# Kernel tuning notes

Measured on AMD Instinct MI355X. Metric: run time of the kernel, lower is better.

## Reference

```python
import jax, jax.numpy as jnp
import numpy as np

B, S, H = 8, 4096, 512
I = 1024
E = 8
TOP_K = 2


def setup_inputs() -> dict:
    key = jax.random.key(0)
    k1, k2, k3, k4, k5 = jax.random.split(key, 5)
    scale_h = 1.0 / np.sqrt(H)
    scale_i = 1.0 / np.sqrt(I)
    return {
        "hidden_states": jax.random.normal(k1, (B, S, H), dtype=jnp.float32),
        "w_router": jax.random.normal(k2, (E, H), dtype=jnp.float32) * scale_h,
        "w_gate": jax.random.normal(k3, (E, I, H), dtype=jnp.float32) * scale_h,
        "w_up": jax.random.normal(k4, (E, I, H), dtype=jnp.float32) * scale_h,
        "w_down": jax.random.normal(k5, (E, H, I), dtype=jnp.float32) * scale_i,
    }


def reference(hidden_states, w_router, w_gate, w_up, w_down):
    dt = hidden_states.dtype
    # Router: logits [B,S,E]
    router_logits = jnp.einsum("bsh,eh->bse", hidden_states, w_router)
    top_vals, top_idx = jax.lax.top_k(router_logits, TOP_K)  # [B,S,K]
    top_w = jax.nn.softmax(top_vals, axis=-1)                # [B,S,K]
    # one-hot over experts: [B,S,K,E]
    oh = jax.nn.one_hot(top_idx, E, dtype=dt)
    combine = jnp.einsum("bsk,bske->bse", top_w, oh)         # per-expert weight per token

    # Faithful to the original: every expert processes the full token batch,
    # result is weighted by the (mostly-zero) combine weights.
    output = jnp.zeros_like(hidden_states)
    for e in range(E):  # fixed small expert count
        g = jnp.einsum("bsh,ih->bsi", hidden_states, w_gate[e])
        u = jnp.einsum("bsh,ih->bsi", hidden_states, w_up[e])
        eo = jnp.einsum("bsi,hi->bsh", jax.nn.silu(g) * u, w_down[e])
        output = output + eo * combine[..., e][..., None]

    # Aux load-balancing loss
    router_probs = jax.nn.softmax(router_logits, axis=-1).mean(axis=(0, 1))  # [E]
    usage = oh.sum(axis=(0, 1, 2))                                           # counts [E]
    usage = usage / jnp.maximum(usage.sum(), 1.0)
    aux_loss = (router_probs * usage).sum() * float(E)
    return output, aux_loss
```

## Files before the change

kernel.cpp:

```cpp
#include <hip/hip_runtime.h>
#include <hip/hip_bf16.h>
#include <math.h>

#define Bb 8
#define Ss 4096
#define Hh 512
#define Ii 1024
#define Ee 8
#define NTOK (Bb*Ss)
#define TT 32
#define IC 128
#define KS 16
#define NBUCKET 64


#define FMA4(acc, s, b) { (acc).x += (s)*(b).x; (acc).y += (s)*(b).y; (acc).z += (s)*(b).z; (acc).w += (s)*(b).w; }

__device__ __forceinline__ float silu_f(float g) {
    return g / (1.0f + expf(-g));
}

__global__ __launch_bounds__(256) void router_kernel(
    const float* __restrict__ hs, const float* __restrict__ wr,
    int* __restrict__ cnt, float* __restrict__ probs_part,
    int* __restrict__ ttok, float* __restrict__ twt)
{
    __shared__ __align__(16) float swr[Ee*Hh];
    __shared__ float sblk[Ee];
    int tid = threadIdx.x;
    for (int q = tid; q < Ee*Hh/4; q += 256)
        ((float4*)swr)[q] = ((const float4*)wr)[q];
    if (tid < Ee) sblk[tid] = 0.0f;
    __syncthreads();

    int lane = tid & 63;
    int t = blockIdx.x*4 + (tid >> 6);
    const float4* h4 = (const float4*)(hs + (size_t)t*Hh);

    float acc[Ee];
    #pragma unroll
    for (int e = 0; e < Ee; e++) acc[e] = 0.0f;
    #pragma unroll
    for (int r = 0; r < 2; r++) {
        float4 hv = h4[lane + 64*r];
        #pragma unroll
        for (int e = 0; e < Ee; e++) {
            float4 wv = ((const float4*)swr)[e*(Hh/4) + lane + 64*r];
            acc[e] += hv.x*wv.x + hv.y*wv.y + hv.z*wv.z + hv.w*wv.w;
        }
    }
    #pragma unroll
    for (int e = 0; e < Ee; e++) {
        #pragma unroll
        for (int off = 32; off > 0; off >>= 1)
            acc[e] += __shfl_xor(acc[e], off);
    }

    if (lane == 0) {
        float m = acc[0];
        #pragma unroll
        for (int e = 1; e < Ee; e++) m = fmaxf(m, acc[e]);
        float p[Ee], s = 0.0f;
        #pragma unroll
        for (int e = 0; e < Ee; e++) { p[e] = expf(acc[e]-m); s += p[e]; }
        float inv = 1.0f/s;
        #pragma unroll
        for (int e = 0; e < Ee; e++) atomicAdd(&sblk[e], p[e]*inv);

        int e0 = 0; float v0 = acc[0];
        #pragma unroll
        for (int e = 1; e < Ee; e++) if (acc[e] > v0) { v0 = acc[e]; e0 = e; }
        int e1 = -1; float v1 = -1e30f;
        #pragma unroll
        for (int e = 0; e < Ee; e++) if (e != e0 && acc[e] > v1) { v1 = acc[e]; e1 = e; }
        float r1 = expf(v1 - v0);
        float w0 = 1.0f/(1.0f + r1);
        float w1 = r1*w0;
        int p0 = atomicAdd(&cnt[e0], 1);
        ttok[e0*NTOK + p0] = t; twt[e0*NTOK + p0] = w0;
        int p1 = atomicAdd(&cnt[e1], 1);
        ttok[e1*NTOK + p1] = t; twt[e1*NTOK + p1] = w1;
    }
    __syncthreads();
    if (tid < Ee)
        atomicAdd(&probs_part[(blockIdx.x & (NBUCKET-1))*Ee + tid], sblk[tid]);
}

__global__ void aux_kernel(const int* __restrict__ cnt,
                           const float* __restrict__ probs_part,
                           float* __restrict__ out_aux)
{
    if (threadIdx.x == 0 && blockIdx.x == 0) {
        float aux = 0.0f;
        for (int e = 0; e < Ee; e++) {
            float ps = 0.0f;
            for (int b = 0; b < NBUCKET; b++) ps += probs_part[b*Ee + e];
            aux += (ps/(float)NTOK) * ((float)cnt[e]/(float)(2*NTOK));
        }
        out_aux[0] = aux * (float)Ee;
    }
}

__global__ __launch_bounds__(256)
__attribute__((amdgpu_waves_per_eu(1, 3)))
void expert_kernel(
    const float* __restrict__ hs,
    const float* __restrict__ wg, const float* __restrict__ wu,
    const float* __restrict__ wd,
    const int* __restrict__ cnt, const int* __restrict__ ttok,
    const float* __restrict__ twt,
    float* __restrict__ out)
{
    int e  = blockIdx.x & (Ee-1);
    int bx = blockIdx.x >> 3;
    int n = cnt[e];
    int j0 = bx * TT;
    if (j0 >= n) return;

    __shared__ __align__(16) float smem[IC*TT + KS*Hh];
    __shared__ int   sm_tok[TT];
    __shared__ float sm_wt[TT];
    float* sm_act = smem;
    float* sm_hT  = smem + IC*TT;
    float* sm_wgT = smem + IC*TT + KS*TT;
    float* sm_wuT = smem + IC*TT + KS*TT + KS*IC;
    float* sm_wdT = smem + IC*TT;

    int tid = threadIdx.x;
    if (tid < TT) {
        int j = j0 + tid;
        int tk; float w;
        if (j < n) { tk = ttok[e*NTOK + j]; w = twt[e*NTOK + j]; }
        else       { tk = ttok[e*NTOK + j0]; w = 0.0f; }
        sm_tok[tid] = tk; sm_wt[tid] = w;
    }
    __syncthreads();

    const float* wg_e = wg + (size_t)e*Ii*Hh;
    const float* wu_e = wu + (size_t)e*Ii*Hh;
    const float* wd_e = wd + (size_t)e*Hh*Ii;

    int t0 = (tid >> 5) * 4;
    int x0 = (tid & 31) * 4;

    int t_h = (tid >> 2) & (TT-1);
    int kq  = (tid & 3) << 2;
    const float* hrow_base = hs + (size_t)sm_tok[t_h]*Hh + kq;
    float* sm_hT_st = sm_hT + kq*TT + t_h;
    int il = tid & 127;
    int kb = (tid >> 7) << 3;
    float* sm_wgT_st = sm_wgT + kb*IC + il;
    float* sm_wuT_st = sm_wuT + kb*IC + il;
    int hh = tid << 1;
    const float* wd_row0 = wd_e + (size_t)hh*Ii;
    const float* wd_row1 = wd_row0 + Ii;
    float* sm_wdT_st = sm_wdT + hh;

    float4 acc_out[4][4];
    #pragma unroll
    for (int a = 0; a < 4; a++)
        #pragma unroll
        for (int b = 0; b < 4; b++)
            acc_out[a][b] = make_float4(0.f, 0.f, 0.f, 0.f);

    for (int ic = 0; ic < Ii; ic += IC) {
        float4 accg[4], accu[4];
        #pragma unroll
        for (int a = 0; a < 4; a++) { accg[a] = make_float4(0,0,0,0); accu[a] = make_float4(0,0,0,0); }

        const float* hp = hrow_base;
        const float* gp = wg_e + (size_t)(ic + il)*Hh + kb;
        const float* up = wu_e + (size_t)(ic + il)*Hh + kb;

        float4 hv = make_float4(0,0,0,0), g0, g1, u0, u1;
        if (tid < 128) hv = *(const float4*)hp;
        g0 = *(const float4*)gp;       g1 = *(const float4*)(gp + 4);
        u0 = *(const float4*)up;       u1 = *(const float4*)(up + 4);

        for (int ks = 0; ks < Hh; ks += KS) {
            if (tid < 128) {
                sm_hT_st[0*TT] = hv.x; sm_hT_st[1*TT] = hv.y;
                sm_hT_st[2*TT] = hv.z; sm_hT_st[3*TT] = hv.w;
            }
            sm_wgT_st[0*IC] = g0.x; sm_wgT_st[1*IC] = g0.y;
            sm_wgT_st[2*IC] = g0.z; sm_wgT_st[3*IC] = g0.w;
            sm_wgT_st[4*IC] = g1.x; sm_wgT_st[5*IC] = g1.y;
            sm_wgT_st[6*IC] = g1.z; sm_wgT_st[7*IC] = g1.w;
            sm_wuT_st[0*IC] = u0.x; sm_wuT_st[1*IC] = u0.y;
            sm_wuT_st[2*IC] = u0.z; sm_wuT_st[3*IC] = u0.w;
            sm_wuT_st[4*IC] = u1.x; sm_wuT_st[5*IC] = u1.y;
            sm_wuT_st[6*IC] = u1.z; sm_wuT_st[7*IC] = u1.w;
            __syncthreads();

            if (ks + KS < Hh) {
                hp += KS; gp += KS; up += KS;
                if (tid < 128) hv = *(const float4*)hp;
                g0 = *(const float4*)gp;   g1 = *(const float4*)(gp + 4);
                u0 = *(const float4*)up;   u1 = *(const float4*)(up + 4);
            }

            #pragma unroll
            for (int k = 0; k < KS; k++) {
                float4 a  = *(const float4*)&sm_hT [k*TT + t0];
                float4 bg = *(const float4*)&sm_wgT[k*IC + x0];
                float4 bu = *(const float4*)&sm_wuT[k*IC + x0];
                FMA4(accg[0], a.x, bg); FMA4(accg[1], a.y, bg);
                FMA4(accg[2], a.z, bg); FMA4(accg[3], a.w, bg);
                FMA4(accu[0], a.x, bu); FMA4(accu[1], a.y, bu);
                FMA4(accu[2], a.z, bu); FMA4(accu[3], a.w, bu);
            }
            __syncthreads();
        }

        {
            float4 v;
            v.x = silu_f(accg[0].x)*accu[0].x; v.y = silu_f(accg[1].x)*accu[1].x;
            v.z = silu_f(accg[2].x)*accu[2].x; v.w = silu_f(accg[3].x)*accu[3].x;
            *(float4*)&sm_act[(x0+0)*TT + t0] = v;
            v.x = silu_f(accg[0].y)*accu[0].y; v.y = silu_f(accg[1].y)*accu[1].y;
            v.z = silu_f(accg[2].y)*accu[2].y; v.w = silu_f(accg[3].y)*accu[3].y;
            *(float4*)&sm_act[(x0+1)*TT + t0] = v;
            v.x = silu_f(accg[0].z)*accu[0].z; v.y = silu_f(accg[1].z)*accu[1].z;
            v.z = silu_f(accg[2].z)*accu[2].z; v.w = silu_f(accg[3].z)*accu[3].z;
            *(float4*)&sm_act[(x0+2)*TT + t0] = v;
            v.x = silu_f(accg[0].w)*accu[0].w; v.y = silu_f(accg[1].w)*accu[1].w;
            v.z = silu_f(accg[2].w)*accu[2].w; v.w = silu_f(accg[3].w)*accu[3].w;
            *(float4*)&sm_act[(x0+3)*TT + t0] = v;
        }
        __syncthreads();

        float4 c0[2][4];
        {
            const float* s0 = wd_row0 + ic;
            const float* s1 = wd_row1 + ic;
            #pragma unroll
            for (int q = 0; q < 4; q++) {
                c0[0][q] = *(const float4*)(s0 + 4*q);
                c0[1][q] = *(const float4*)(s1 + 4*q);
            }
        }
        for (int ks2 = 0; ks2 < IC; ks2 += KS) {
            #pragma unroll
            for (int rr = 0; rr < 2; rr++) {
                float* st = sm_wdT_st + rr;
                st[ 0*Hh] = c0[rr][0].x; st[ 1*Hh] = c0[rr][0].y;
                st[ 2*Hh] = c0[rr][0].z; st[ 3*Hh] = c0[rr][0].w;
                st[ 4*Hh] = c0[rr][1].x; st[ 5*Hh] = c0[rr][1].y;
                st[ 6*Hh] = c0[rr][1].z; st[ 7*Hh] = c0[rr][1].w;
                st[ 8*Hh] = c0[rr][2].x; st[ 9*Hh] = c0[rr][2].y;
                st[10*Hh] = c0[rr][2].z; st[11*Hh] = c0[rr][2].w;
                st[12*Hh] = c0[rr][3].x; st[13*Hh] = c0[rr][3].y;
                st[14*Hh] = c0[rr][3].z; st[15*Hh] = c0[rr][3].w;
            }
            __syncthreads();

            if (ks2 + KS < IC) {
                const float* s0 = wd_row0 + ic + ks2 + KS;
                const float* s1 = wd_row1 + ic + ks2 + KS;
                #pragma unroll
                for (int q = 0; q < 4; q++) {
                    c0[0][q] = *(const float4*)(s0 + 4*q);
                    c0[1][q] = *(const float4*)(s1 + 4*q);
                }
            }

            #pragma unroll
            for (int k = 0; k < KS; k++) {
                float4 av = *(const float4*)&sm_act[(ks2+k)*TT + t0];
                #pragma unroll
                for (int j = 0; j < 4; j++) {
                    float4 b = *(const float4*)&sm_wdT[k*Hh + x0 + 128*j];
                    FMA4(acc_out[0][j], av.x, b);
                    FMA4(acc_out[1][j], av.y, b);
                    FMA4(acc_out[2][j], av.z, b);
                    FMA4(acc_out[3][j], av.w, b);
                }
            }
            __syncthreads();
        }
    }

    #pragma unroll
    for (int tj = 0; tj < 4; tj++) {
        float w = sm_wt[t0 + tj];
        size_t base = (size_t)sm_tok[t0 + tj]*Hh;
        #pragma unroll
        for (int j = 0; j < 4; j++) {
            float4 v = acc_out[tj][j];
            atomicAdd(&out[base + x0 + 128*j + 0], v.x*w);
            atomicAdd(&out[base + x0 + 128*j + 1], v.y*w);
            atomicAdd(&out[base + x0 + 128*j + 2], v.z*w);
            atomicAdd(&out[base + x0 + 128*j + 3], v.w*w);
        }
    }
}

extern "C" void kernel_launch(void* const* d_in, const int* in_sizes, int n_in,
                              void* d_out, int out_size, void* d_ws, size_t ws_size,
                              hipStream_t stream) {
    const float* hs = (const float*)d_in[0];
    const float* wr = (const float*)d_in[1];
    const float* wg = (const float*)d_in[2];
    const float* wu = (const float*)d_in[3];
    const float* wd = (const float*)d_in[4];
    float* out = (float*)d_out;

    int*   cnt   = (int*)d_ws;
    float* probs = (float*)((char*)d_ws + 64);
    int*   ttok  = (int*)((char*)d_ws + 4096);
    float* twt   = (float*)((char*)d_ws + 4096 + sizeof(int)*(size_t)Ee*NTOK);

    hipMemsetAsync(d_out, 0, (size_t)(NTOK*Hh + 1)*sizeof(float), stream);
    hipMemsetAsync(d_ws, 0, 4096, stream);

    router_kernel<<<NTOK/4, 256, 0, stream>>>(hs, wr, cnt, probs, ttok, twt);
    aux_kernel<<<1, 64, 0, stream>>>(cnt, probs, out + (size_t)NTOK*Hh);

    int tiles = (NTOK + TT - 1)/TT;
    expert_kernel<<<tiles*Ee, 256, 0, stream>>>(hs, wg, wu, wd, cnt, ttok, twt, out);
}
```

Baseline: 5.189 ms.

## Replace FP32 FMA expert path with split-bf16 MFMA grouped GEMMs

Splits the activations and the expert weights into hi/lo bf16 planes and runs the expert FFN as two grouped GEMM kernels built on 32x32x16 bf16 MFMA. Each product uses three MFMAs (hi*hi, lo*hi, hi*lo) to approximate fp32 accuracy. The intermediate silu(g)*u activations go to a padded, per-expert-prefixed workspace buffer instead of being recomputed inside a fused kernel. The aim is to move the matmul work off scalar FP32 FMAs and onto the matrix cores. The cost is extra split passes over the weights every call, a large workspace, and an activation round-trip through global memory, with a fallback to the old kernel when the workspace is too small.

```diff
diff --git a/kernel.cpp b/kernel.cpp
--- a/kernel.cpp
+++ b/kernel.cpp
@@ -8,11 +8,42 @@
 #define Ii 1024
 #define Ee 8
 #define NTOK (Bb*Ss)
+#define NBUCKET 64
+
 #define TT 32
 #define IC 128
 #define KS 16
-#define NBUCKET 64
-
+
+#define BM 64
+#define BN 256
+#define BK 32
+#define LDK 40
+
+typedef short  bf16x8 __attribute__((ext_vector_type(8)));
+typedef float  f32x16 __attribute__((ext_vector_type(16)));
+#define MFMA32(a,b,c) __builtin_amdgcn_mfma_f32_32x32x16_bf16((a),(b),(c),0,0,0)
+#define ZERO16 {0.f,0.f,0.f,0.f,0.f,0.f,0.f,0.f,0.f,0.f,0.f,0.f,0.f,0.f,0.f,0.f}
+
+#define WS_CNT     0
+#define WS_PROBS   64
+#define WS_PREFIX  4096
+#define WS_TTOK    8192ull
+#define WS_TWT     (WS_TTOK + 4ull*Ee*NTOK)
+#define WS_PLANES  (WS_TWT + 4ull*Ee*NTOK)
+#define HS_N   ((size_t)NTOK*Hh)
+#define WE_N   ((size_t)Ee*Ii*Hh)
+#define WS_HS_HI   WS_PLANES
+#define WS_HS_LO   (WS_HS_HI + 2ull*HS_N)
+#define WS_WG_HI   (WS_HS_LO + 2ull*HS_N)
+#define WS_WG_LO   (WS_WG_HI + 2ull*WE_N)
+#define WS_WU_HI   (WS_WG_LO + 2ull*WE_N)
+#define WS_WU_LO   (WS_WU_HI + 2ull*WE_N)
+#define WS_WD_HI   (WS_WU_LO + 2ull*WE_N)
+#define WS_WD_LO   (WS_WD_HI + 2ull*WE_N)
+#define ACT_ROWS   66560ull
+#define WS_ACT_HI  (WS_WD_LO + 2ull*WE_N)
+#define WS_ACT_LO  (WS_ACT_HI + 2ull*ACT_ROWS*Ii)
+#define WS_NEED    (WS_ACT_LO + 2ull*ACT_ROWS*Ii)
 
 #define FMA4(acc, s, b) { (acc).x += (s)*(b).x; (acc).y += (s)*(b).y; (acc).z += (s)*(b).z; (acc).w += (s)*(b).w; }
 
@@ -88,16 +119,320 @@
 
 __global__ void aux_kernel(const int* __restrict__ cnt,
                            const float* __restrict__ probs_part,
-                           float* __restrict__ out_aux)
+                           float* __restrict__ out_aux,
+                           int* __restrict__ prefix)
 {
     if (threadIdx.x == 0 && blockIdx.x == 0) {
         float aux = 0.0f;
+        int acc = 0;
         for (int e = 0; e < Ee; e++) {
             float ps = 0.0f;
             for (int b = 0; b < NBUCKET; b++) ps += probs_part[b*Ee + e];
             aux += (ps/(float)NTOK) * ((float)cnt[e]/(float)(2*NTOK));
+            prefix[e] = acc;
+            acc += ((cnt[e] + 63) >> 6) << 6;
         }
         out_aux[0] = aux * (float)Ee;
+        prefix[8] = acc;
+    }
+}
+
+__global__ __launch_bounds__(256) void split_kernel(
+    const float* __restrict__ src, ushort* __restrict__ hi, ushort* __restrict__ lo, int n4)
+{
+    int idx = blockIdx.x*256 + threadIdx.x;
+    if (idx >= n4) return;
+    float4 f = ((const float4*)src)[idx];
+    ushort h[4], l[4];
+    #pragma unroll
+    for (int j = 0; j < 4; j++) {
+        float fv = ((const float*)&f)[j];
+        unsigned u = __float_as_uint(fv);
+        unsigned r = (u + 0x7fffu + ((u>>16)&1u)) & 0xffff0000u;
+        h[j] = (ushort)(r >> 16);
+        float lof = fv - __uint_as_float(r);
+        l[j] = (ushort)(__float_as_uint(lof) >> 16);
+    }
+    ((ushort4*)hi)[idx] = make_ushort4(h[0], h[1], h[2], h[3]);
+    ((ushort4*)lo)[idx] = make_ushort4(l[0], l[1], l[2], l[3]);
+}
+
+__global__ __launch_bounds__(256)
+__attribute__((amdgpu_waves_per_eu(1, 2)))
+void gemm1_kernel(const ushort* __restrict__ hs_hi, const ushort* __restrict__ hs_lo,
+                  const ushort* __restrict__ wg_hi, const ushort* __restrict__ wg_lo,
+                  const ushort* __restrict__ wu_hi, const ushort* __restrict__ wu_lo,
+                  const int* __restrict__ cnt, const int* __restrict__ prefix,
+                  const int* __restrict__ ttok,
+                  ushort* __restrict__ act_hi, ushort* __restrict__ act_lo)
+{
+    const int e  = blockIdx.x & 7;
+    const int rr = blockIdx.x >> 3;
+    const int mt = rr & 511;
+    const int it = rr >> 9;
+    const int n  = cnt[e];
+    const int j0 = mt * BM;
+    if (j0 >= n) return;
+    const int abase = prefix[e] + j0;
+    const int ic = it * 128;
+
+    __shared__ __align__(16) ushort sA[2][BM*LDK];
+    __shared__ __align__(16) ushort sB[2][BN*LDK];
+    __shared__ int sm_tok[BM];
+
+    const int tid = threadIdx.x;
+    if (tid < BM) {
+        int j = j0 + tid;
+        sm_tok[tid] = ttok[e*NTOK + (j < n ? j : j0)];
+    }
+    __syncthreads();
+
+    const int srow = tid >> 2;
+    const int sch  = tid & 3;
+    const int sxch = (sch ^ ((srow >> 3) & 3)) * 8;
+    const ushort* aph = hs_hi + (size_t)sm_tok[srow]*Hh + sch*8;
+    const ushort* apl = hs_lo + (size_t)sm_tok[srow]*Hh + sch*8;
+    const int a_st = srow*LDK + sxch;
+
+    const ushort* wgh_e = wg_hi + (size_t)e*Ii*Hh;
+    const ushort* wgl_e = wg_lo + (size_t)e*Ii*Hh;
+    const ushort* wuh_e = wu_hi + (size_t)e*Ii*Hh;
+    const ushort* wul_e = wu_lo + (size_t)e*Ii*Hh;
+    const ushort* bph[4];
+    const ushort* bpl[4];
+    bph[0] = wgh_e + (size_t)(ic +      srow)*Hh + sch*8;
+    bpl[0] = wgl_e + (size_t)(ic +      srow)*Hh + sch*8;
+    bph[1] = wgh_e + (size_t)(ic + 64 + srow)*Hh + sch*8;
+    bpl[1] = wgl_e + (size_t)(ic + 64 + srow)*Hh + sch*8;
+    bph[2] = wuh_e + (size_t)(ic +      srow)*Hh + sch*8;
+    bpl[2] = wul_e + (size_t)(ic +      srow)*Hh + sch*8;
+    bph[3] = wuh_e + (size_t)(ic + 64 + srow)*Hh + sch*8;
+    bpl[3] = wul_e + (size_t)(ic + 64 + srow)*Hh + sch*8;
+    int b_st[4];
+    #pragma unroll
+    for (int c = 0; c < 4; c++) b_st[c] = (c*64 + srow)*LDK + sxch;
+
+    const int w   = tid >> 6;
+    const int l31 = tid & 31;
+    const int g   = (tid >> 5) & 1;
+    const int axr = (l31 >> 3) & 3;
+    const int ck0 = ((g    ) ^ axr) * 8;
+    const int ck1 = ((g + 2) ^ axr) * 8;
+    const int arow0 = (     l31)*LDK;
+    const int arow1 = (32 + l31)*LDK;
+    const int brow_g = ((w  )*32 + l31)*LDK;
+    const int brow_u = ((w+4)*32 + l31)*LDK;
+
+    f32x16 accg0 = ZERO16, accg1 = ZERO16, accu0 = ZERO16, accu1 = ZERO16;
+
+    bf16x8 ra_h = *(const bf16x8*)aph;
+    bf16x8 ra_l = *(const bf16x8*)apl;
+    bf16x8 rb_h[4], rb_l[4];
+    #pragma unroll
+    for (int c = 0; c < 4; c++) { rb_h[c] = *(const bf16x8*)bph[c]; rb_l[c] = *(const bf16x8*)bpl[c]; }
+
+    for (int ks = 0; ks < Hh/BK; ks++) {
+        *(bf16x8*)&sA[0][a_st] = ra_h;
+        *(bf16x8*)&sA[1][a_st] = ra_l;
+        #pragma unroll
+        for (int c = 0; c < 4; c++) {
+            *(bf16x8*)&sB[0][b_st[c]] = rb_h[c];
+            *(bf16x8*)&sB[1][b_st[c]] = rb_l[c];
+        }
+        __syncthreads();
+
+        if (ks + 1 < Hh/BK) {
+            aph += BK; apl += BK;
+            ra_h = *(const bf16x8*)aph; ra_l = *(const bf16x8*)apl;
+            #pragma unroll
+            for (int c = 0; c < 4; c++) {
+                bph[c] += BK; bpl[c] += BK;
+                rb_h[c] = *(const bf16x8*)bph[c];
+                rb_l[c] = *(const bf16x8*)bpl[c];
+            }
+        }
+
+        #pragma unroll
+        for (int kk = 0; kk < 2; kk++) {
+            const int ck = kk ? ck1 : ck0;
+            bf16x8 a0h = *(const bf16x8*)&sA[0][arow0 + ck];
+            bf16x8 a0l = *(const bf16x8*)&sA[1][arow0 + ck];
+            bf16x8 a1h = *(const bf16x8*)&sA[0][arow1 + ck];
+            bf16x8 a1l = *(const bf16x8*)&sA[1][arow1 + ck];
+            bf16x8 bgh = *(const bf16x8*)&sB[0][brow_g + ck];
+            bf16x8 bgl = *(const bf16x8*)&sB[1][brow_g + ck];
+            bf16x8 buh = *(const bf16x8*)&sB[0][brow_u + ck];
+            bf16x8 bul = *(const bf16x8*)&sB[1][brow_u + ck];
+            accg0 = MFMA32(a0h, bgh, accg0);
+            accg0 = MFMA32(a0l, bgh, accg0);
+            accg0 = MFMA32(a0h, bgl, accg0);
+            accu0 = MFMA32(a0h, buh, accu0);
+            accu0 = MFMA32(a0l, buh, accu0);
+            accu0 = MFMA32(a0h, bul, accu0);
+            accg1 = MFMA32(a1h, bgh, accg1);
+            accg1 = MFMA32(a1l, bgh, accg1);
+            accg1 = MFMA32(a1h, bgl, accg1);
+            accu1 = MFMA32(a1h, buh, accu1);
+            accu1 = MFMA32(a1l, buh, accu1);
+            accu1 = MFMA32(a1h, bul, accu1);
+        }
+        __syncthreads();
+    }
+
+    const int icol = ic + w*32 + l31;
+    #pragma unroll
+    for (int r = 0; r < 16; r++) {
+        int m = (r&3) + 8*(r>>2) + 4*g;
+        {
+            float a = silu_f(accg0[r]) * accu0[r];
+            size_t off = (size_t)(abase + m)*Ii + icol;
+            unsigned u = __float_as_uint(a);
+            unsigned rh = (u + 0x7fffu + ((u>>16)&1u)) & 0xffff0000u;
+            act_hi[off] = (ushort)(rh >> 16);
+            float lof = a - __uint_as_float(rh);
+            act_lo[off] = (ushort)(__float_as_uint(lof) >> 16);
+        }
+        {
+            float a = silu_f(accg1[r]) * accu1[r];
+            size_t off = (size_t)(abase + 32 + m)*Ii + icol;
+            unsigned u = __float_as_uint(a);
+            unsigned rh = (u + 0x7fffu + ((u>>16)&1u)) & 0xffff0000u;
+            act_hi[off] = (ushort)(rh >> 16);
+            float lof = a - __uint_as_float(rh);
+            act_lo[off] = (ushort)(__float_as_uint(lof) >> 16);
+        }
+    }
+}
+
+__global__ __launch_bounds__(256)
+__attribute__((amdgpu_waves_per_eu(1, 2)))
+void gemm2_kernel(const ushort* __restrict__ act_hi, const ushort* __restrict__ act_lo,
+                  const ushort* __restrict__ wd_hi, const ushort* __restrict__ wd_lo,
+                  const int* __restrict__ cnt, const int* __restrict__ prefix,
+                  const int* __restrict__ ttok, const float* __restrict__ twt,
+                  float* __restrict__ out)
+{
+    const int e  = blockIdx.x & 7;
+    const int rr = blockIdx.x >> 3;
+    const int mt = rr & 511;
+    const int ht = rr >> 9;
+    const int n  = cnt[e];
+    const int j0 = mt * BM;
+    if (j0 >= n) return;
+    const int abase = prefix[e] + j0;
+    const int hbase = ht * 256;
+
+    __shared__ __align__(16) ushort sA[2][BM*LDK];
+    __shared__ __align__(16) ushort sB[2][BN*LDK];
+    __shared__ int   sm_tok[BM];
+    __shared__ float sm_wt[BM];
+
+    const int tid = threadIdx.x;
+    if (tid < BM) {
+        int j = j0 + tid;
+        if (j < n) { sm_tok[tid] = ttok[e*NTOK + j]; sm_wt[tid] = twt[e*NTOK + j]; }
+        else       { sm_tok[tid] = ttok[e*NTOK + j0]; sm_wt[tid] = 0.0f; }
+    }
+    __syncthreads();
+
+    const int srow = tid >> 2;
+    const int sch  = tid & 3;
+    const int sxch = (sch ^ ((srow >> 3) & 3)) * 8;
+    const ushort* aph = act_hi + (size_t)(abase + srow)*Ii + sch*8;
+    const ushort* apl = act_lo + (size_t)(abase + srow)*Ii + sch*8;
+    const int a_st = srow*LDK + sxch;
+
+    const ushort* wdh_e = wd_hi + (size_t)e*Hh*Ii;
+    const ushort* wdl_e = wd_lo + (size_t)e*Hh*Ii;
+    const ushort* bph[4];
+    const ushort* bpl[4];
+    #pragma unroll
+    for (int c = 0; c < 4; c++) {
+        bph[c] = wdh_e + (size_t)(hbase + c*64 + srow)*Ii + sch*8;
+        bpl[c] = wdl_e + (size_t)(hbase + c*64 + srow)*Ii + sch*8;
+    }
+    int b_st[4];
+    #pragma unroll
+    for (int c = 0; c < 4; c++) b_st[c] = (c*64 + srow)*LDK + sxch;
+
+    const int w   = tid >> 6;
+    const int l31 = tid & 31;
+    const int g   = (tid >> 5) & 1;
+    const int axr = (l31 >> 3) & 3;
+    const int ck0 = ((g    ) ^ axr) * 8;
+    const int ck1 = ((g + 2) ^ axr) * 8;
+    const int arow0 = (     l31)*LDK;
+    const int arow1 = (32 + l31)*LDK;
+    const int brow_a = ((w  )*32 + l31)*LDK;
+    const int brow_b = ((w+4)*32 + l31)*LDK;
+
+    f32x16 acc00 = ZERO16, acc01 = ZERO16, acc10 = ZERO16, acc11 = ZERO16;
+
+    bf16x8 ra_h = *(const bf16x8*)aph;
+    bf16x8 ra_l = *(const bf16x8*)apl;
+    bf16x8 rb_h[4], rb_l[4];
+    #pragma unroll
+    for (int c = 0; c < 4; c++) { rb_h[c] = *(const bf16x8*)bph[c]; rb_l[c] = *(const bf16x8*)bpl[c]; }
+
+    for (int ks = 0; ks < Ii/BK; ks++) {
+        *(bf16x8*)&sA[0][a_st] = ra_h;
+        *(bf16x8*)&sA[1][a_st] = ra_l;
+        #pragma unroll
+        for (int c = 0; c < 4; c++) {
+            *(bf16x8*)&sB[0][b_st[c]] = rb_h[c];
+            *(bf16x8*)&sB[1][b_st[c]] = rb_l[c];
+        }
+        __syncthreads();
+
+        if (ks + 1 < Ii/BK) {
+            aph += BK; apl += BK;
+            ra_h = *(const bf16x8*)aph; ra_l = *(const bf16x8*)apl;
+            #pragma unroll
+            for (int c = 0; c < 4; c++) {
+                bph[c] += BK; bpl[c] += BK;
+                rb_h[c] = *(const bf16x8*)bph[c];
+                rb_l[c] = *(const bf16x8*)bpl[c];
+            }
+        }
+
+        #pragma unroll
+        for (int kk = 0; kk < 2; kk++) {
+            const int ck = kk ? ck1 : ck0;
+            bf16x8 a0h = *(const bf16x8*)&sA[0][arow0 + ck];
+            bf16x8 a0l = *(const bf16x8*)&sA[1][arow0 + ck];
+            bf16x8 a1h = *(const bf16x8*)&sA[0][arow1 + ck];
+            bf16x8 a1l = *(const bf16x8*)&sA[1][arow1 + ck];
+            bf16x8 b0h = *(const bf16x8*)&sB[0][brow_a + ck];
+            bf16x8 b0l = *(const bf16x8*)&sB[1][brow_a + ck];
+            bf16x8 b1h = *(const bf16x8*)&sB[0][brow_b + ck];
+            bf16x8 b1l = *(const bf16x8*)&sB[1][brow_b + ck];
+            acc00 = MFMA32(a0h, b0h, acc00);
+            acc00 = MFMA32(a0l, b0h, acc00);
+            acc00 = MFMA32(a0h, b0l, acc00);
+            acc01 = MFMA32(a0h, b1h, acc01);
+            acc01 = MFMA32(a0l, b1h, acc01);
+            acc01 = MFMA32(a0h, b1l, acc01);
+            acc10 = MFMA32(a1h, b0h, acc10);
+            acc10 = MFMA32(a1l, b0h, acc10);
+            acc10 = MFMA32(a1h, b0l, acc10);
+            acc11 = MFMA32(a1h, b1h, acc11);
+            acc11 = MFMA32(a1l, b1h, acc11);
+            acc11 = MFMA32(a1h, b1l, acc11);
+        }
+        __syncthreads();
+    }
+
+    const int h0 = hbase +       w*32 + l31;
+    const int h1 = hbase + 128 + w*32 + l31;
+    #pragma unroll
+    for (int r = 0; r < 16; r++) {
+        int m = (r&3) + 8*(r>>2) + 4*g;
+        int   tok0 = sm_tok[m],      tok1 = sm_tok[32 + m];
+        float wt0  = sm_wt[m],       wt1  = sm_wt[32 + m];
+        atomicAdd(&out[(size_t)tok0*Hh + h0], acc00[r]*wt0);
+        atomicAdd(&out[(size_t)tok0*Hh + h1], acc01[r]*wt0);
+        atomicAdd(&out[(size_t)tok1*Hh + h0], acc10[r]*wt1);
+        atomicAdd(&out[(size_t)tok1*Hh + h1], acc11[r]*wt1);
     }
 }
 
@@ -241,16 +576,16 @@
         }
         for (int ks2 = 0; ks2 < IC; ks2 += KS) {
             #pragma unroll
-            for (int rr = 0; rr < 2; rr++) {
-                float* st = sm_wdT_st + rr;
-                st[ 0*Hh] = c0[rr][0].x; st[ 1*Hh] = c0[rr][0].y;
-                st[ 2*Hh] = c0[rr][0].z; st[ 3*Hh] = c0[rr][0].w;
-                st[ 4*Hh] = c0[rr][1].x; st[ 5*Hh] = c0[rr][1].y;
-                st[ 6*Hh] = c0[rr][1].z; st[ 7*Hh] = c0[rr][1].w;
-                st[ 8*Hh] = c0[rr][2].x; st[ 9*Hh] = c0[rr][2].y;
-                st[10*Hh] = c0[rr][2].z; st[11*Hh] = c0[rr][2].w;
-                st[12*Hh] = c0[rr][3].x; st[13*Hh] = c0[rr][3].y;
-                st[14*Hh] = c0[rr][3].z; st[15*Hh] = c0[rr][3].w;
+            for (int rr2 = 0; rr2 < 2; rr2++) {
+                float* st = sm_wdT_st + rr2;
+                st[ 0*Hh] = c0[rr2][0].x; st[ 1*Hh] = c0[rr2][0].y;
+                st[ 2*Hh] = c0[rr2][0].z; st[ 3*Hh] = c0[rr2][0].w;
+                st[ 4*Hh] = c0[rr2][1].x; st[ 5*Hh] = c0[rr2][1].y;
+                st[ 6*Hh] = c0[rr2][1].z; st[ 7*Hh] = c0[rr2][1].w;
+                st[ 8*Hh] = c0[rr2][2].x; st[ 9*Hh] = c0[rr2][2].y;
+                st[10*Hh] = c0[rr2][2].z; st[11*Hh] = c0[rr2][2].w;
+                st[12*Hh] = c0[rr2][3].x; st[13*Hh] = c0[rr2][3].y;
+                st[14*Hh] = c0[rr2][3].z; st[15*Hh] = c0[rr2][3].w;
             }
             __syncthreads();
 
@@ -305,17 +640,41 @@
     const float* wd = (const float*)d_in[4];
     float* out = (float*)d_out;
 
-    int*   cnt   = (int*)d_ws;
-    float* probs = (float*)((char*)d_ws + 64);
-    int*   ttok  = (int*)((char*)d_ws + 4096);
-    float* twt   = (float*)((char*)d_ws + 4096 + sizeof(int)*(size_t)Ee*NTOK);
-
-    hipMemsetAsync(d_out, 0, (size_t)(NTOK*Hh + 1)*sizeof(float), stream);
-    hipMemsetAsync(d_ws, 0, 4096, stream);
+    char* ws = (char*)d_ws;
+    int*   cnt    = (int*)(ws + WS_CNT);
+    float* probs  = (float*)(ws + WS_PROBS);
+    int*   prefix = (int*)(ws + WS_PREFIX);
+    int*   ttok   = (int*)(ws + WS_TTOK);
+    float* twt    = (float*)(ws + WS_TWT);
+
+    hipMemsetAsync(d_out, 0, ((size_t)NTOK*Hh + 1)*sizeof(float), stream);
+    hipMemsetAsync(d_ws, 0, 4608, stream);
 
     router_kernel<<<NTOK/4, 256, 0, stream>>>(hs, wr, cnt, probs, ttok, twt);
-    aux_kernel<<<1, 64, 0, stream>>>(cnt, probs, out + (size_t)NTOK*Hh);
-
-    int tiles = (NTOK + TT - 1)/TT;
-    expert_kernel<<<tiles*Ee, 256, 0, stream>>>(hs, wg, wu, wd, cnt, ttok, twt, out);
-}
+    aux_kernel<<<1, 64, 0, stream>>>(cnt, probs, out + (size_t)NTOK*Hh, prefix);
+
+    if (ws_size >= WS_NEED) {
+        ushort* hs_hi = (ushort*)(ws + WS_HS_HI);
+        ushort* hs_lo = (ushort*)(ws + WS_HS_LO);
+        ushort* wg_hi = (ushort*)(ws + WS_WG_HI);
+        ushort* wg_lo = (ushort*)(ws + WS_WG_LO);
+        ushort* wu_hi = (ushort*)(ws + WS_WU_HI);
+        ushort* wu_lo = (ushort*)(ws + WS_WU_LO);
+        ushort* wd_hi = (ushort*)(ws + WS_WD_HI);
+        ushort* wd_lo = (ushort*)(ws + WS_WD_LO);
+        ushort* act_hi = (ushort*)(ws + WS_ACT_HI);
+        ushort* act_lo = (ushort*)(ws + WS_ACT_LO);
+
+        split_kernel<<<(int)(HS_N/4/256), 256, 0, stream>>>(hs, hs_hi, hs_lo, (int)(HS_N/4));
+        split_kernel<<<(int)(WE_N/4/256), 256, 0, stream>>>(wg, wg_hi, wg_lo, (int)(WE_N/4));
+        split_kernel<<<(int)(WE_N/4/256), 256, 0, stream>>>(wu, wu_hi, wu_lo, (int)(WE_N/4));
+        split_kernel<<<(int)(WE_N/4/256), 256, 0, stream>>>(wd, wd_hi, wd_lo, (int)(WE_N/4));
+
+        gemm1_kernel<<<8*512*8, 256, 0, stream>>>(hs_hi, hs_lo, wg_hi, wg_lo, wu_hi, wu_lo,
+                                                  cnt, prefix, ttok, act_hi, act_lo);
+        gemm2_kernel<<<8*512*2, 256, 0, stream>>>(act_hi, act_lo, wd_hi, wd_lo,
+                                                  cnt, prefix, ttok, twt, out);
+    } else {
+        expert_kernel<<<1024*8, 256, 0, stream>>>(hs, wg, wu, wd, cnt, ttok, twt, out);
+    }
+}
```

Measured after the change: 5.182 ms. Within noise of the previous version (-0.1%).
